# Kernel tuning notes

Measured on AMD Instinct MI355X. Metric: run time of the kernel, lower is better.

Reference implementation:

```python
import jax, jax.numpy as jnp
import numpy as np

NX, NY, NZ = 128, 128, 8
N_VOX = NX * NY * NZ
V, C, HF, WF = 6, 64, 116, 200
PAD_H, PAD_W = 928.0, 1600.0  # img_pad_shape (input image after padding)
IMG_H, IMG_W = 928.0, 1600.0  # img_shape used for the valid-flag bounds check


def _make_proj_mats():
    # Structured lidar2img matrices: pinhole intrinsics + 6 yaw-distributed cameras.
    K = np.array([[500.0, 0, 400, 0], [0, 500.0, 232, 0], [0, 0, 1, 0], [0, 0, 0, 1]], dtype=np.float64)
    A = np.array([[0.0, -1, 0], [0, 0, -1], [1, 0, 0]], dtype=np.float64)  # lidar(x fwd,y left,z up)->cam(z fwd)
    mats = []
    for j in range(V):
        yaw = 2.0 * np.pi * j / V
        c, s = np.cos(yaw), np.sin(yaw)
        Rz = np.array([[c, s, 0], [-s, c, 0], [0, 0, 1]])
        T = np.eye(4)
        T[:3, :3] = A @ Rz
        T[:3, 3] = np.array([0.0, -1.0, 0.0])
        mats.append(K @ T)
    return jnp.asarray(np.stack(mats), dtype=jnp.float32)


def setup_inputs() -> dict:
    key = jax.random.key(0)
    k1, k2 = jax.random.split(key)
    x_fov = jax.random.normal(k1, (1, V, C, HF, WF), dtype=jnp.float32)
    lo = jnp.array([-50.0, -50.0, -5.0], jnp.float32)
    span = jnp.array([100.0, 100.0, 8.0], jnp.float32)
    points = jax.random.uniform(k2, (N_VOX, 3), dtype=jnp.float32) * span + lo
    proj_mats = _make_proj_mats()
    return {"x_fov": x_fov, "points": points, "proj_mats": proj_mats}


def _bilinear_sample(feat, px, py):
    # feat [C,HF,WF]; px/py [N] in feature-map pixel coords.
    # Matches F.grid_sample(mode='bilinear', padding_mode='zeros', align_corners=False).
    x0 = jnp.floor(px)
    y0 = jnp.floor(py)
    wx1 = px - x0
    wy1 = py - y0

    def gather(xi, yi, w):
        inb = (xi >= 0) & (xi < WF) & (yi >= 0) & (yi < HF)
        xc = jnp.clip(xi, 0, WF - 1).astype(jnp.int32)
        yc = jnp.clip(yi, 0, HF - 1).astype(jnp.int32)
        return feat[:, yc, xc] * (w * inb)[None, :]  # [C,N]

    return (gather(x0, y0, (1 - wx1) * (1 - wy1))
            + gather(x0 + 1, y0, wx1 * (1 - wy1))
            + gather(x0, y0 + 1, (1 - wx1) * wy1)
            + gather(x0 + 1, y0 + 1, wx1 * wy1))


def _forward(x_fov, points, proj_mats):
    n = points.shape[0]
    # points_cam2img: homogeneous projection, perspective divide
    pts_h = jnp.concatenate([points, jnp.ones((n, 1), points.dtype)], axis=-1)  # [N,4]
    cam = jnp.einsum('vij,nj->vni', proj_mats, pts_h)  # [V,N,4]
    depth = cam[..., 2]
    d_safe = jnp.where(jnp.abs(depth) > 1e-6, depth, 1e-6)
    u = cam[..., 0] / d_safe  # image-plane x in input-image pixels (scale=1, crop=0, no flip)
    v = cam[..., 1] / d_safe
    # valid_flag: in front of camera and inside img_shape
    valid = (depth > 0) & (u > 0) & (u < IMG_W) & (v > 0) & (v < IMG_H)  # [V,N]
    # normalize by img_pad_shape then map to feature-map pixels (align_corners=False)
    px = u / PAD_W * WF - 0.5
    py = v / PAD_H * HF - 0.5
    feats = jax.vmap(_bilinear_sample)(x_fov[0], px, py)  # [V,C,N]
    feats = feats * valid[:, None, :].astype(feats.dtype)
    vol = feats.sum(0)  # [C,N] masked sum over views
    cnt = valid.sum(0).astype(feats.dtype)  # [N]
    vol = jnp.where(cnt > 0, vol, 0.0) / jnp.clip(cnt, 0.001)[None, :]
    # reshape(n_voxels[::-1] + [-1]).permute(3,2,1,0) -> [C,NX,NY,NZ]
    out = jnp.transpose(vol.reshape(C, NZ, NY, NX), (0, 3, 2, 1))
    return out[None]  # [1,C,NX,NY,NZ]


def reference(x_fov, points, proj_mats):
    return _forward(x_fov, points, proj_mats)
```

## Files before the change

### kernel.cpp

```cpp
#include <hip/hip_runtime.h>
#include <hip/hip_bf16.h>
#include <hip/hip_fp16.h>

#define NXv 128
#define NYv 128
#define NZv 8
#define NVOX (NXv * NYv * NZv)
#define NV 6
#define NC 64
#define HFv 116
#define WFv 200
#define PLANE (HFv * WFv)

#define FT_BYTES   ((size_t)NV * PLANE * NC * 2)
#define PD_BYTES   ((size_t)NVOX * NV * 16)
#define INVC_BYTES ((size_t)NVOX * 4)

__device__ inline unsigned short f2bf(float f) {
  unsigned int x = __float_as_uint(f);
  unsigned int r = x + 0x7fffu + ((x >> 16) & 1u);
  return (unsigned short)(r >> 16);
}
__device__ inline float bf_lo(unsigned int q) { return __uint_as_float(q << 16); }
__device__ inline float bf_hi(unsigned int q) { return __uint_as_float(q & 0xffff0000u); }

__device__ inline unsigned short f2h_bits(float f) {
  __half h = __float2half(f);
  return *reinterpret_cast<unsigned short*>(&h);
}
__device__ inline float h_bits2f(unsigned short u) {
  __half_raw r; r.x = u;
  __half h = *reinterpret_cast<__half*>(&r);
  return __half2float(h);
}

__global__ __launch_bounds__(256) void transpose_feat_bf16(
    const float* __restrict__ in, unsigned int* __restrict__ out32) {
  __shared__ float tile[64][65];
  const int v  = blockIdx.y;
  const int p0 = blockIdx.x * 64;
  const float* src = in + (size_t)v * NC * PLANE;
  unsigned int* dst = out32 + (size_t)v * PLANE * (NC / 2);
  const int t = threadIdx.x;

#pragma unroll
  for (int i = 0; i < 4; ++i) {
    const int idx = i * 256 + t;
    const int c  = idx >> 4;
    const int p4 = idx & 15;
    const int pp = p0 + p4 * 4;
    if (pp < PLANE) {
      const float4 f = *(const float4*)(src + (size_t)c * PLANE + pp);
      tile[p4 * 4 + 0][c] = f.x;
      tile[p4 * 4 + 1][c] = f.y;
      tile[p4 * 4 + 2][c] = f.z;
      tile[p4 * 4 + 3][c] = f.w;
    }
  }
  __syncthreads();

#pragma unroll
  for (int i = 0; i < 8; ++i) {
    const int idx = i * 256 + t;
    const int p   = idx >> 5;
    const int c2  = idx & 31;
    const int pp  = p0 + p;
    if (pp < PLANE) {
      const unsigned int lo = f2bf(tile[p][c2 * 2 + 0]);
      const unsigned int hi = f2bf(tile[p][c2 * 2 + 1]);
      dst[(size_t)pp * 32 + c2] = lo | (hi << 16);
    }
  }
}

__global__ __launch_bounds__(256) void precompute_proj(
    const float* __restrict__ points,
    const float* __restrict__ proj,
    uint4* __restrict__ pdata_r,
    float* __restrict__ invc_r) {
  const int n = blockIdx.x * 256 + threadIdx.x;
  const float x = points[n * 3 + 0];
  const float y = points[n * 3 + 1];
  const float z = points[n * 3 + 2];

  const int iz  = n >> 14;
  const int rem = n & 16383;
  const int iy  = rem >> 7;
  const int ix  = rem & 127;
  const int rp  = ((iy >> 3) * 128 + ix) * 64 + ((iy & 7) * 8 + iz);

  float cnt = 0.0f;

#pragma unroll
  for (int v = 0; v < NV; ++v) {
    const float* M = proj + v * 16;
    const float cx = M[0] * x + M[1] * y + M[2]  * z + M[3];
    const float cy = M[4] * x + M[5] * y + M[6]  * z + M[7];
    const float cz = M[8] * x + M[9] * y + M[10] * z + M[11];

    const float dz = (fabsf(cz) > 1e-6f) ? cz : 1e-6f;
    const float u  = cx / dz;
    const float vv = cy / dz;

    const bool valid = (cz > 0.0f) && (u > 0.0f) && (u < 1600.0f) &&
                       (vv > 0.0f) && (vv < 928.0f);
    cnt += valid ? 1.0f : 0.0f;

    const float px = u  / 1600.0f * 200.0f - 0.5f;
    const float py = vv / 928.0f  * 116.0f - 0.5f;
    const float fx0 = floorf(px);
    const float fy0 = floorf(py);
    const float wx1 = px - fx0;
    const float wy1 = py - fy0;
    const float wx0 = 1.0f - wx1;
    const float wy0 = 1.0f - wy1;
    const int ix0 = (int)fx0;
    const int iy0 = (int)fy0;

    unsigned int pix[4];
    unsigned short wh[4];
    const int   xs[4] = {ix0, ix0 + 1, ix0,     ix0 + 1};
    const int   ys[4] = {iy0, iy0,     iy0 + 1, iy0 + 1};
    const float ww[4] = {wx0 * wy0, wx1 * wy0, wx0 * wy1, wx1 * wy1};
#pragma unroll
    for (int k = 0; k < 4; ++k) {
      const int xi = xs[k], yi = ys[k];
      const bool inb = (xi >= 0) && (xi < WFv) && (yi >= 0) && (yi < HFv);
      const int xc = min(max(xi, 0), WFv - 1);
      const int yc = min(max(yi, 0), HFv - 1);
      pix[k] = (unsigned int)(yc * WFv + xc);
      wh[k]  = f2h_bits((inb && valid) ? ww[k] : 0.0f);
    }

    uint4 rec;
    rec.x = pix[0] | (valid ? 0x8000u : 0u) | (pix[1] << 16);
    rec.y = pix[2] | (pix[3] << 16);
    rec.z = (unsigned int)wh[0] | ((unsigned int)wh[1] << 16);
    rec.w = (unsigned int)wh[2] | ((unsigned int)wh[3] << 16);
    pdata_r[(size_t)rp * NV + v] = rec;
  }
  invc_r[rp] = (cnt > 0.0f) ? (1.0f / cnt) : 0.0f;
}

__global__ __launch_bounds__(256) void gather_kernel(
    const unsigned int* __restrict__ feat32,
    const uint4* __restrict__ pdata_r,
    const float* __restrict__ invc_r,
    float* __restrict__ out) {
  __shared__ float tile[64][65];
  __shared__ uint4 pdl[64 * NV];
  __shared__ float invl[64];

  const int b    = blockIdx.x;
  const int ix   = b & 127;
  const int iy0g = (b >> 7) << 3;
  const int t    = threadIdx.x;
  const int lane = t & 63;
  const int wave = t >> 6;
  const int half = lane >> 5;
  const int c2   = lane & 31;

  {
    const uint4* src = pdata_r + (size_t)b * 64 * NV;
    for (int i = t; i < 64 * NV; i += 256) pdl[i] = src[i];
    if (t < 64) invl[t] = invc_r[(size_t)b * 64 + t];
  }
  __syncthreads();

#pragma unroll 1
  for (int k = 0; k < 8; ++k) {
    const int sl = wave * 16 + k * 2 + half;
    float accx = 0.0f, accy = 0.0f;

#pragma unroll
    for (int v = 0; v < NV; ++v) {
      const uint4 rec = pdl[sl * NV + v];
      const bool vld = (rec.x & 0x8000u) != 0;
      if (vld) {
        const unsigned int p00 = rec.x & 0x7fffu;
        const unsigned int p10 = rec.x >> 16;
        const unsigned int p01 = rec.y & 0xffffu;
        const unsigned int p11 = rec.y >> 16;
        const float w0 = h_bits2f((unsigned short)(rec.z & 0xffffu));
        const float w1 = h_bits2f((unsigned short)(rec.z >> 16));
        const float w2 = h_bits2f((unsigned short)(rec.w & 0xffffu));
        const float w3 = h_bits2f((unsigned short)(rec.w >> 16));

        const unsigned int* fb = feat32 + (size_t)v * PLANE * 32 + c2;
        const unsigned int q0 = fb[(size_t)p00 * 32];
        const unsigned int q1 = fb[(size_t)p10 * 32];
        const unsigned int q2 = fb[(size_t)p01 * 32];
        const unsigned int q3 = fb[(size_t)p11 * 32];

        accx = fmaf(w0, bf_lo(q0), accx);  accy = fmaf(w0, bf_hi(q0), accy);
        accx = fmaf(w1, bf_lo(q1), accx);  accy = fmaf(w1, bf_hi(q1), accy);
        accx = fmaf(w2, bf_lo(q2), accx);  accy = fmaf(w2, bf_hi(q2), accy);
        accx = fmaf(w3, bf_lo(q3), accx);  accy = fmaf(w3, bf_hi(q3), accy);
      }
    }

    const float inv = invl[sl];
    tile[sl][c2 * 2 + 0] = accx * inv;
    tile[sl][c2 * 2 + 1] = accy * inv;
  }

  __syncthreads();

  const size_t obase = (size_t)ix * (NYv * NZv) + (size_t)iy0g * NZv + lane;
#pragma unroll
  for (int i = 0; i < 16; ++i) {
    const int c = i * 4 + wave;
    out[(size_t)c * NVOX + obase] = tile[lane][c];
  }
}

__global__ __launch_bounds__(256) void sample_fallback(
    const float* __restrict__ feat,
    const float* __restrict__ points,
    const float* __restrict__ proj,
    float* __restrict__ out) {
  const int wave = threadIdx.x >> 6;
  const int lane = threadIdx.x & 63;
  const int n = blockIdx.x * 4 + wave;

  const float x = points[n * 3 + 0];
  const float y = points[n * 3 + 1];
  const float z = points[n * 3 + 2];

  float acc = 0.0f;
  int cnt = 0;

#pragma unroll
  for (int v = 0; v < NV; ++v) {
    const float* M = proj + v * 16;
    const float cx = M[0] * x + M[1] * y + M[2]  * z + M[3];
    const float cy = M[4] * x + M[5] * y + M[6]  * z + M[7];
    const float cz = M[8] * x + M[9] * y + M[10] * z + M[11];
    const float dz = (fabsf(cz) > 1e-6f) ? cz : 1e-6f;
    const float u  = cx / dz;
    const float vv = cy / dz;
    const bool valid = (cz > 0.0f) && (u > 0.0f) && (u < 1600.0f) &&
                       (vv > 0.0f) && (vv < 928.0f);
    if (!valid) continue;
    cnt++;
    const float px = u  / 1600.0f * 200.0f - 0.5f;
    const float py = vv / 928.0f  * 116.0f - 0.5f;
    const float fx0 = floorf(px);
    const float fy0 = floorf(py);
    const float wx1 = px - fx0;
    const float wy1 = py - fy0;
    const float wx0 = 1.0f - wx1;
    const float wy0 = 1.0f - wy1;
    const int ix0 = (int)fx0;
    const int iy0 = (int)fy0;
    const float w00 = wx0 * wy0, w10 = wx1 * wy0, w01 = wx0 * wy1, w11 = wx1 * wy1;
    const float* basev = feat + ((size_t)v * NC + lane) * PLANE;
    auto tap = [&](int xi, int yi, float w) {
      if (xi >= 0 && xi < WFv && yi >= 0 && yi < HFv)
        acc += w * basev[yi * WFv + xi];
    };
    tap(ix0,     iy0,     w00);
    tap(ix0 + 1, iy0,     w10);
    tap(ix0,     iy0 + 1, w01);
    tap(ix0 + 1, iy0 + 1, w11);
  }

  const float scale = (cnt > 0) ? (1.0f / (float)cnt) : 0.0f;
  const int iz  = n >> 14;
  const int rem = n & 16383;
  const int iy  = rem >> 7;
  const int ixx = rem & 127;
  out[(((size_t)lane * NXv + ixx) * NYv + iy) * NZv + iz] = acc * scale;
}

extern "C" void kernel_launch(void* const* d_in, const int* in_sizes, int n_in,
                              void* d_out, int out_size, void* d_ws, size_t ws_size,
                              hipStream_t stream) {
  const float* x_fov  = (const float*)d_in[0];
  const float* points = (const float*)d_in[1];
  const float* proj   = (const float*)d_in[2];
  float* out = (float*)d_out;

  if (ws_size >= FT_BYTES + PD_BYTES + INVC_BYTES) {
    unsigned int* ft = (unsigned int*)d_ws;
    uint4* pd = (uint4*)((char*)d_ws + FT_BYTES);
    float* ic = (float*)((char*)d_ws + FT_BYTES + PD_BYTES);

    dim3 tgrid((PLANE + 63) / 64, NV);
    transpose_feat_bf16<<<tgrid, 256, 0, stream>>>(x_fov, ft);
    precompute_proj<<<NVOX / 256, 256, 0, stream>>>(points, proj, pd, ic);
    gather_kernel<<<NXv * NYv / 8, 256, 0, stream>>>(ft, pd, ic, out);
  } else {
    sample_fallback<<<NVOX / 4, 256, 0, stream>>>(x_fov, points, proj, out);
  }
}
```

Baseline: 123.2 us.

## Fuse projection precompute into gather kernel and widen feature loads to 16 bytes

Removes the separate precompute_proj kernel and its global pdata/invc round trip. Each gather block now projects its own 64 voxels into shared memory, counting valid views with shared atomics. The gather loop now has each lane load a uint4 of 8 bf16 channels per corner instead of one 32-bit word, so each lane holds 8 accumulators. The transpose kernel also writes uint2 instead of uint32. The trade is some per-block projection work, shared atomics and higher register pressure, in exchange for one fewer launch and less global traffic.

```diff
diff --git a/kernel.cpp b/kernel.cpp
--- a/kernel.cpp
+++ b/kernel.cpp
@@ -12,9 +12,7 @@
 #define WFv 200
 #define PLANE (HFv * WFv)
 
-#define FT_BYTES   ((size_t)NV * PLANE * NC * 2)
-#define PD_BYTES   ((size_t)NVOX * NV * 16)
-#define INVC_BYTES ((size_t)NVOX * 4)
+#define FT_BYTES ((size_t)NV * PLANE * NC * 2)
 
 __device__ inline unsigned short f2bf(float f) {
   unsigned int x = __float_as_uint(f);
@@ -60,40 +58,55 @@
   __syncthreads();
 
 #pragma unroll
-  for (int i = 0; i < 8; ++i) {
+  for (int i = 0; i < 4; ++i) {
     const int idx = i * 256 + t;
-    const int p   = idx >> 5;
-    const int c2  = idx & 31;
+    const int p   = idx >> 4;
+    const int c4  = idx & 15;
     const int pp  = p0 + p;
     if (pp < PLANE) {
-      const unsigned int lo = f2bf(tile[p][c2 * 2 + 0]);
-      const unsigned int hi = f2bf(tile[p][c2 * 2 + 1]);
-      dst[(size_t)pp * 32 + c2] = lo | (hi << 16);
+      uint2 w;
+      w.x = (unsigned int)f2bf(tile[p][c4 * 4 + 0]) |
+            ((unsigned int)f2bf(tile[p][c4 * 4 + 1]) << 16);
+      w.y = (unsigned int)f2bf(tile[p][c4 * 4 + 2]) |
+            ((unsigned int)f2bf(tile[p][c4 * 4 + 3]) << 16);
+      *(uint2*)(dst + (size_t)pp * 32 + c4 * 2) = w;
     }
   }
 }
 
-__global__ __launch_bounds__(256) void precompute_proj(
+__global__ __launch_bounds__(256) void gather_fused(
+    const uint4* __restrict__ feat4,
     const float* __restrict__ points,
     const float* __restrict__ proj,
-    uint4* __restrict__ pdata_r,
-    float* __restrict__ invc_r) {
-  const int n = blockIdx.x * 256 + threadIdx.x;
-  const float x = points[n * 3 + 0];
-  const float y = points[n * 3 + 1];
-  const float z = points[n * 3 + 2];
-
-  const int iz  = n >> 14;
-  const int rem = n & 16383;
-  const int iy  = rem >> 7;
-  const int ix  = rem & 127;
-  const int rp  = ((iy >> 3) * 128 + ix) * 64 + ((iy & 7) * 8 + iz);
-
-  float cnt = 0.0f;
-
-#pragma unroll
-  for (int v = 0; v < NV; ++v) {
-    const float* M = proj + v * 16;
+    float* __restrict__ out) {
+  __shared__ float tile[64][65];
+  __shared__ uint4 pdl[64 * NV];
+  __shared__ float invl[64];
+  __shared__ float projl[96];
+
+  const int b    = blockIdx.x;
+  const int ix   = b & 127;
+  const int iy0g = (b >> 7) << 3;
+  const int t    = threadIdx.x;
+  const int lane = t & 63;
+  const int wave = t >> 6;
+
+  if (t < 96) projl[t] = proj[t];
+  if (t < 64) invl[t] = 0.0f;
+  __syncthreads();
+
+  for (int task = t; task < 64 * NV; task += 256) {
+    const int slot = task / NV;
+    const int v    = task - slot * NV;
+    const int j    = slot >> 3;
+    const int iz   = slot & 7;
+    const int n    = iz * (NXv * NYv) + (iy0g + j) * NXv + ix;
+
+    const float x = points[n * 3 + 0];
+    const float y = points[n * 3 + 1];
+    const float z = points[n * 3 + 2];
+
+    const float* M = projl + v * 16;
     const float cx = M[0] * x + M[1] * y + M[2]  * z + M[3];
     const float cy = M[4] * x + M[5] * y + M[6]  * z + M[7];
     const float cz = M[8] * x + M[9] * y + M[10] * z + M[11];
@@ -104,7 +117,7 @@
 
     const bool valid = (cz > 0.0f) && (u > 0.0f) && (u < 1600.0f) &&
                        (vv > 0.0f) && (vv < 928.0f);
-    cnt += valid ? 1.0f : 0.0f;
+    if (valid) atomicAdd(&invl[slot], 1.0f);
 
     const float px = u  / 1600.0f * 200.0f - 0.5f;
     const float py = vv / 928.0f  * 116.0f - 0.5f;
@@ -137,46 +150,26 @@
     rec.y = pix[2] | (pix[3] << 16);
     rec.z = (unsigned int)wh[0] | ((unsigned int)wh[1] << 16);
     rec.w = (unsigned int)wh[2] | ((unsigned int)wh[3] << 16);
-    pdata_r[(size_t)rp * NV + v] = rec;
-  }
-  invc_r[rp] = (cnt > 0.0f) ? (1.0f / cnt) : 0.0f;
-}
-
-__global__ __launch_bounds__(256) void gather_kernel(
-    const unsigned int* __restrict__ feat32,
-    const uint4* __restrict__ pdata_r,
-    const float* __restrict__ invc_r,
-    float* __restrict__ out) {
-  __shared__ float tile[64][65];
-  __shared__ uint4 pdl[64 * NV];
-  __shared__ float invl[64];
-
-  const int b    = blockIdx.x;
-  const int ix   = b & 127;
-  const int iy0g = (b >> 7) << 3;
-  const int t    = threadIdx.x;
-  const int lane = t & 63;
-  const int wave = t >> 6;
-  const int half = lane >> 5;
-  const int c2   = lane & 31;
-
-  {
-    const uint4* src = pdata_r + (size_t)b * 64 * NV;
-    for (int i = t; i < 64 * NV; i += 256) pdl[i] = src[i];
-    if (t < 64) invl[t] = invc_r[(size_t)b * 64 + t];
-  }
-  __syncthreads();
-
-#pragma unroll 1
-  for (int k = 0; k < 8; ++k) {
-    const int sl = wave * 16 + k * 2 + half;
-    float accx = 0.0f, accy = 0.0f;
+    pdl[slot * NV + v] = rec;
+  }
+  __syncthreads();
+  if (t < 64) { const float c = invl[t]; invl[t] = (c > 0.0f) ? 1.0f / c : 0.0f; }
+  __syncthreads();
+
+  const int pg = lane >> 3;
+  const int ch = lane & 7;
+
+#pragma unroll
+  for (int it = 0; it < 2; ++it) {
+    const int sl = wave * 16 + it * 8 + pg;
+    float acc[8];
+#pragma unroll
+    for (int j2 = 0; j2 < 8; ++j2) acc[j2] = 0.0f;
 
 #pragma unroll
     for (int v = 0; v < NV; ++v) {
       const uint4 rec = pdl[sl * NV + v];
-      const bool vld = (rec.x & 0x8000u) != 0;
-      if (vld) {
+      if (rec.x & 0x8000u) {
         const unsigned int p00 = rec.x & 0x7fffu;
         const unsigned int p10 = rec.x >> 16;
         const unsigned int p01 = rec.y & 0xffffu;
@@ -186,22 +179,37 @@
         const float w2 = h_bits2f((unsigned short)(rec.w & 0xffffu));
         const float w3 = h_bits2f((unsigned short)(rec.w >> 16));
 
-        const unsigned int* fb = feat32 + (size_t)v * PLANE * 32 + c2;
-        const unsigned int q0 = fb[(size_t)p00 * 32];
-        const unsigned int q1 = fb[(size_t)p10 * 32];
-        const unsigned int q2 = fb[(size_t)p01 * 32];
-        const unsigned int q3 = fb[(size_t)p11 * 32];
-
-        accx = fmaf(w0, bf_lo(q0), accx);  accy = fmaf(w0, bf_hi(q0), accy);
-        accx = fmaf(w1, bf_lo(q1), accx);  accy = fmaf(w1, bf_hi(q1), accy);
-        accx = fmaf(w2, bf_lo(q2), accx);  accy = fmaf(w2, bf_hi(q2), accy);
-        accx = fmaf(w3, bf_lo(q3), accx);  accy = fmaf(w3, bf_hi(q3), accy);
+        const uint4* fb = feat4 + (size_t)v * PLANE * 8 + ch;
+        const uint4 q0 = fb[(size_t)p00 * 8];
+        const uint4 q1 = fb[(size_t)p10 * 8];
+        const uint4 q2 = fb[(size_t)p01 * 8];
+        const uint4 q3 = fb[(size_t)p11 * 8];
+
+        acc[0] = fmaf(w0, bf_lo(q0.x), acc[0]); acc[1] = fmaf(w0, bf_hi(q0.x), acc[1]);
+        acc[2] = fmaf(w0, bf_lo(q0.y), acc[2]); acc[3] = fmaf(w0, bf_hi(q0.y), acc[3]);
+        acc[4] = fmaf(w0, bf_lo(q0.z), acc[4]); acc[5] = fmaf(w0, bf_hi(q0.z), acc[5]);
+        acc[6] = fmaf(w0, bf_lo(q0.w), acc[6]); acc[7] = fmaf(w0, bf_hi(q0.w), acc[7]);
+
+        acc[0] = fmaf(w1, bf_lo(q1.x), acc[0]); acc[1] = fmaf(w1, bf_hi(q1.x), acc[1]);
+        acc[2] = fmaf(w1, bf_lo(q1.y), acc[2]); acc[3] = fmaf(w1, bf_hi(q1.y), acc[3]);
+        acc[4] = fmaf(w1, bf_lo(q1.z), acc[4]); acc[5] = fmaf(w1, bf_hi(q1.z), acc[5]);
+        acc[6] = fmaf(w1, bf_lo(q1.w), acc[6]); acc[7] = fmaf(w1, bf_hi(q1.w), acc[7]);
+
+        acc[0] = fmaf(w2, bf_lo(q2.x), acc[0]); acc[1] = fmaf(w2, bf_hi(q2.x), acc[1]);
+        acc[2] = fmaf(w2, bf_lo(q2.y), acc[2]); acc[3] = fmaf(w2, bf_hi(q2.y), acc[3]);
+        acc[4] = fmaf(w2, bf_lo(q2.z), acc[4]); acc[5] = fmaf(w2, bf_hi(q2.z), acc[5]);
+        acc[6] = fmaf(w2, bf_lo(q2.w), acc[6]); acc[7] = fmaf(w2, bf_hi(q2.w), acc[7]);
+
+        acc[0] = fmaf(w3, bf_lo(q3.x), acc[0]); acc[1] = fmaf(w3, bf_hi(q3.x), acc[1]);
+        acc[2] = fmaf(w3, bf_lo(q3.y), acc[2]); acc[3] = fmaf(w3, bf_hi(q3.y), acc[3]);
+        acc[4] = fmaf(w3, bf_lo(q3.z), acc[4]); acc[5] = fmaf(w3, bf_hi(q3.z), acc[5]);
+        acc[6] = fmaf(w3, bf_lo(q3.w), acc[6]); acc[7] = fmaf(w3, bf_hi(q3.w), acc[7]);
       }
     }
 
     const float inv = invl[sl];
-    tile[sl][c2 * 2 + 0] = accx * inv;
-    tile[sl][c2 * 2 + 1] = accy * inv;
+#pragma unroll
+    for (int j2 = 0; j2 < 8; ++j2) tile[sl][ch * 8 + j2] = acc[j2] * inv;
   }
 
   __syncthreads();
@@ -281,15 +289,11 @@
   const float* proj   = (const float*)d_in[2];
   float* out = (float*)d_out;
 
-  if (ws_size >= FT_BYTES + PD_BYTES + INVC_BYTES) {
+  if (ws_size >= FT_BYTES) {
     unsigned int* ft = (unsigned int*)d_ws;
-    uint4* pd = (uint4*)((char*)d_ws + FT_BYTES);
-    float* ic = (float*)((char*)d_ws + FT_BYTES + PD_BYTES);
-
     dim3 tgrid((PLANE + 63) / 64, NV);
     transpose_feat_bf16<<<tgrid, 256, 0, stream>>>(x_fov, ft);
-    precompute_proj<<<NVOX / 256, 256, 0, stream>>>(points, proj, pd, ic);
-    gather_kernel<<<NXv * NYv / 8, 256, 0, stream>>>(ft, pd, ic, out);
+    gather_fused<<<NXv * NYv / 8, 256, 0, stream>>>((const uint4*)ft, points, proj, out);
   } else {
     sample_fallback<<<NVOX / 4, 256, 0, stream>>>(x_fov, points, proj, out);
   }
```

After: 109.4 us. -11.2%, faster.
